# Performance work log

Hardware: AMD Instinct MI355X
Metric: run time of the kernel (lower is better)

## Reference

```python
import jax, jax.numpy as jnp
import numpy as np
from jax.ops import segment_sum

N_NODES = 50000
N_EDGES = 800000
NUM_FEAT = 16
EDGE_DIM = 8
H = 100
L = 2
BN_EPS = 1e-5


def setup_inputs() -> dict:
    key = jax.random.key(0)
    ks = iter(jax.random.split(key, 40))
    def w(shape, scale=0.05):
        return (jax.random.normal(next(ks), shape, dtype=jnp.float32) * scale)
    inp = {
        "x": jax.random.normal(next(ks), (N_NODES, NUM_FEAT), dtype=jnp.float32),
        "edge_index": jax.random.randint(next(ks), (2, N_EDGES), 0, N_NODES, dtype=jnp.int64) if jax.config.jax_enable_x64 else jax.random.randint(next(ks), (2, N_EDGES), 0, N_NODES).astype(jnp.int32),
        "edge_attr": jax.random.normal(next(ks), (N_EDGES, EDGE_DIM), dtype=jnp.float32),
        # embeddings
        "node_w": w((NUM_FEAT, H)), "node_b": w((H,)),
        "edge_w": w((EDGE_DIM, H)), "edge_b": w((H,)),
        # per-layer GINEConv MLP (stacked over layers)
        "conv_w1": w((L, H, H)), "conv_b1": w((L, H)),
        "conv_w2": w((L, H, H)), "conv_b2": w((L, H)),
        # batchnorm affine params
        "bn_gamma": jnp.ones((L, H), dtype=jnp.float32), "bn_beta": jnp.zeros((L, H), dtype=jnp.float32),
        # per-layer edge-update MLP
        "emlp_w1": w((L, 3 * H, H)), "emlp_b1": w((L, H)),
        "emlp_w2": w((L, H, H)), "emlp_b2": w((L, H)),
        # final classifier MLP (3H -> 50 -> 25 -> 2); dropout is identity at eval
        "mlp_w1": w((3 * H, 50)), "mlp_b1": w((50,)),
        "mlp_w2": w((50, 25)), "mlp_b2": w((25,)),
        "mlp_w3": w((25, 2)), "mlp_b3": w((2,)),
    }
    return inp


def reference(x, edge_index, edge_attr,
              node_w, node_b, edge_w, edge_b,
              conv_w1, conv_b1, conv_w2, conv_b2,
              bn_gamma, bn_beta,
              emlp_w1, emlp_b1, emlp_w2, emlp_b2,
              mlp_w1, mlp_b1, mlp_w2, mlp_b2, mlp_w3, mlp_b3):
    src, dst = edge_index[0], edge_index[1]
    n_nodes = x.shape[0]

    h = x @ node_w + node_b          # [N, H]
    e = edge_attr @ edge_w + edge_b  # [E, H]

    for i in range(L):
        # GINEConv: out_i = nn((1+eps)*h_i + sum_{e: dst=i} relu(h_src + e)); eps=0
        msg = jax.nn.relu(h[src] + e)                       # [E, H] gather + combine
        agg = segment_sum(msg, dst, num_segments=n_nodes)   # [N, H] scatter-add
        z = h + agg
        z = jax.nn.relu(z @ conv_w1[i] + conv_b1[i]) @ conv_w2[i] + conv_b2[i]
        # BatchNorm (train mode: batch stats over nodes, biased variance)
        mu = jnp.mean(z, axis=0)
        var = jnp.var(z, axis=0)
        z = (z - mu) * jax.lax.rsqrt(var + BN_EPS) * bn_gamma[i] + bn_beta[i]
        h = (h + jax.nn.relu(z)) * 0.5
        # edge update: e += MLP([h_src, h_dst, e]) / 2
        cat = jnp.concatenate([h[src], h[dst], e], axis=-1)  # [E, 3H]
        upd = jax.nn.relu(cat @ emlp_w1[i] + emlp_b1[i]) @ emlp_w2[i] + emlp_b2[i]
        e = e + upd * 0.5

    # per-edge features: relu([h_src, h_dst]) ++ e  -> [E, 3H]
    feat = jnp.concatenate([jax.nn.relu(jnp.concatenate([h[src], h[dst]], axis=-1)), e], axis=-1)
    out = jax.nn.relu(feat @ mlp_w1 + mlp_b1)
    out = jax.nn.relu(out @ mlp_w2 + mlp_b2)
    return out @ mlp_w3 + mlp_b3  # [E, 2]
```

## Files before the change

kernel.cpp:

```cpp
#include <hip/hip_runtime.h>
#include <hip/hip_bf16.h>

#define N_NODES 50000
#define N_EDGES 800000
#define HDIM 100
#define ESTR 104

typedef _Float16 half8_t __attribute__((ext_vector_type(8)));
typedef _Float16 half4_t __attribute__((ext_vector_type(4)));
typedef float f32x4_t __attribute__((ext_vector_type(4)));

struct FragDesc {
  const float* src; int stride; int K; int N; int outOff; int ksteps; int ntiles;
};
struct PrepArgs {
  FragDesc d[20];
  int prefix[21];
  int ndesc;
};

__global__ void k_prep_frags(PrepArgs args, _Float16* __restrict__ out) {
  int b = blockIdx.x;
  int di = 0;
  while (di + 1 < args.ndesc && b >= args.prefix[di + 1]) di++;
  FragDesc d = args.d[di];
  int local = b - args.prefix[di];
  int t = local / d.ksteps;
  int s = local % d.ksteps;
  int lane = threadIdx.x;
  int col = t * 16 + (lane & 15);
  int kb = s * 32 + (lane >> 4) * 8;
  _Float16* o = out + d.outOff + (size_t)((t * d.ksteps + s) * 64 + lane) * 8;
  #pragma unroll
  for (int i = 0; i < 8; ++i) {
    int k = kb + i;
    float v = (k < d.K && col < d.N) ? d.src[(size_t)k * d.stride + col] : 0.0f;
    o[i] = (_Float16)v;
  }
}

__global__ void k_ws_probe(float* out, float mb) { out[0] = mb; }

__global__ void k_hist(const int* __restrict__ dst, int* __restrict__ cnt) {
  for (int e = blockIdx.x * blockDim.x + threadIdx.x; e < N_EDGES;
       e += gridDim.x * blockDim.x)
    atomicAdd(&cnt[dst[e]], 1);
}

__global__ __launch_bounds__(1024) void k_scan(const int* cnt,
                                               int* rowptr,
                                               int* cursor) {
  __shared__ int part[1024];
  int t = threadIdx.x;
  const int CH = (N_NODES + 1023) / 1024;
  int base = t * CH;
  int s = 0;
  for (int i = 0; i < CH; ++i) {
    int n = base + i;
    if (n < N_NODES) s += cnt[n];
  }
  part[t] = s;
  __syncthreads();
  for (int off = 1; off < 1024; off <<= 1) {
    int v = 0;
    if (t >= off) v = part[t - off];
    __syncthreads();
    if (t >= off) part[t] += v;
    __syncthreads();
  }
  int run = (t == 0) ? 0 : part[t - 1];
  for (int i = 0; i < CH; ++i) {
    int n = base + i;
    if (n <= N_NODES) {
      rowptr[n] = run;
      if (n < N_NODES) {
        int cv = cnt[n];
        cursor[n] = run;
        run += cv;
      }
    }
  }
}

__global__ void k_perm(const int* __restrict__ src, const int* __restrict__ dst,
                       int* __restrict__ cursor, int* __restrict__ perm,
                       int* __restrict__ srcS, int* __restrict__ dstS) {
  for (int e = blockIdx.x * blockDim.x + threadIdx.x; e < N_EDGES;
       e += gridDim.x * blockDim.x) {
    int d = dst[e];
    int pos = atomicAdd(&cursor[d], 1);
    perm[pos] = e;
    srcS[pos] = src[e];
    dstS[pos] = d;
  }
}

template<bool L0>
__global__ __launch_bounds__(256) void k_agg(
    const int* __restrict__ rowptr, const int* __restrict__ perm,
    const int* __restrict__ srcS,
    const float* __restrict__ attr, const float* __restrict__ ew,
    const float* __restrict__ ebias,
    const _Float16* __restrict__ e,
    const float* __restrict__ h, float* __restrict__ agg) {
  __shared__ float EwL[800];
  __shared__ float ebL[128];
  int tid = threadIdx.x;
  if constexpr (L0) {
    for (int idx = tid; idx < 800; idx += 256) EwL[idx] = ew[idx];
    if (tid < 128) ebL[tid] = (tid < HDIM) ? ebias[tid] : 0.0f;
    __syncthreads();
  }
  int n = blockIdx.x * 2 + (tid >> 7);
  int j = tid & 127;
  if (n >= N_NODES || j >= HDIM) return;
  float acc = 0.0f;
  int p0 = rowptr[n], p1 = rowptr[n + 1];
  for (int pos = p0; pos < p1; ++pos) {
    int s = srcS[pos];
    float m;
    if constexpr (L0) {
      int eid = perm[pos];
      const float* ap = attr + (size_t)eid * 8;
      float e0 = ebL[j];
      #pragma unroll
      for (int k = 0; k < 8; ++k) e0 += ap[k] * EwL[k * HDIM + j];
      m = h[(size_t)s * HDIM + j] + e0;
    } else {
      m = h[(size_t)s * HDIM + j] + (float)e[(size_t)pos * ESTR + j];
    }
    acc += fmaxf(m, 0.0f);
  }
  agg[(size_t)n * HDIM + j] = acc;
}

__device__ __forceinline__ half8_t h8_zero() {
  half8_t a;
  #pragma unroll
  for (int i = 0; i < 8; ++i) a[i] = (_Float16)0.0f;
  return a;
}

__device__ __forceinline__ int swz_idx(int r, int c) {
  int chunk = (c >> 3) ^ (r & 7);
  return r * 128 + chunk * 8 + (c & 7);
}

template<int MODE>
__device__ __forceinline__ void load_a_node(const float* hp0,
                                            const float* ap0,
                                            int row, int lane, half8_t av[4]) {
  int g = lane >> 4;
  bool rv = (row < N_NODES);
  const float* hp = hp0 + (size_t)row * HDIM;
  const float* ap = ap0 + (size_t)row * HDIM;
  #pragma unroll
  for (int s = 0; s < 4; ++s) {
    int kb = s * 32 + g * 8;
    half8_t a = h8_zero();
    if (rv && kb < HDIM) {
      float f[8];
      #pragma unroll
      for (int i = 0; i < 8; ++i) f[i] = 0.0f;
      if (kb + 8 <= HDIM) {
        float4 v0 = *(const float4*)(hp + kb);
        float4 v1 = *(const float4*)(hp + kb + 4);
        f[0] = v0.x; f[1] = v0.y; f[2] = v0.z; f[3] = v0.w;
        f[4] = v1.x; f[5] = v1.y; f[6] = v1.z; f[7] = v1.w;
        if constexpr (MODE == 2) {
          float4 u0 = *(const float4*)(ap + kb);
          float4 u1 = *(const float4*)(ap + kb + 4);
          f[0] += u0.x; f[1] += u0.y; f[2] += u0.z; f[3] += u0.w;
          f[4] += u1.x; f[5] += u1.y; f[6] += u1.z; f[7] += u1.w;
        }
      } else {
        float4 v0 = *(const float4*)(hp + kb);
        f[0] = v0.x; f[1] = v0.y; f[2] = v0.z; f[3] = v0.w;
        if constexpr (MODE == 2) {
          float4 u0 = *(const float4*)(ap + kb);
          f[0] += u0.x; f[1] += u0.y; f[2] += u0.z; f[3] += u0.w;
        }
      }
      #pragma unroll
      for (int i = 0; i < 8; ++i) {
        float v = f[i];
        if constexpr (MODE == 1) v = fmaxf(v, 0.0f);
        a[i] = (_Float16)v;
      }
    }
    av[s] = a;
  }
}

template<int NT, int KS>
__device__ __forceinline__ void mfma_tiles(const half8_t* av, const _Float16* __restrict__ fb,
                                           int lane, f32x4_t* acc) {
  #pragma unroll
  for (int t = 0; t < NT; ++t) {
    #pragma unroll
    for (int s = 0; s < KS; ++s) {
      half8_t bv = *(const half8_t*)(fb + (size_t)(((t * KS + s) * 64 + lane) << 3));
      acc[t] = __builtin_amdgcn_mfma_f32_16x16x32_f16(av[s], bv, acc[t], 0, 0, 0);
    }
  }
}

template<int KS>
__device__ __forceinline__ void lds_read_a(const _Float16* L, int lane, half8_t* av) {
  int r = lane & 15;
  int g = lane >> 4;
  #pragma unroll
  for (int s = 0; s < KS; ++s) {
    int kb = s * 32 + g * 8;
    av[s] = *(const half8_t*)&L[swz_idx(r, kb)];
  }
}

__global__ void k_embed_h(const float* __restrict__ x, const float* __restrict__ w,
                          const float* __restrict__ bias, float* __restrict__ h) {
  int n = blockIdx.x;
  int j = threadIdx.x;
  if (j >= HDIM) return;
  float acc = bias[j];
  #pragma unroll
  for (int k = 0; k < 16; ++k) acc += x[n * 16 + k] * w[k * HDIM + j];
  h[(size_t)n * HDIM + j] = acc;
}

__global__ __launch_bounds__(256) void k_node_conv(
    const float* __restrict__ h, const float* agg,
    const _Float16* __restrict__ fb1, const _Float16* __restrict__ fb2,
    const float* __restrict__ b1, const float* __restrict__ b2,
    float* z, float* __restrict__ bn_sum, float* __restrict__ bn_sq) {
  __shared__ __align__(16) _Float16 lds[4][2048];
  int lane = threadIdx.x & 63;
  int wave = threadIdx.x >> 6;
  _Float16* L = lds[wave];
  int mbase = (blockIdx.x * 4 + wave) * 16;

  half8_t av[4];
  load_a_node<2>(h, agg, mbase + (lane & 15), lane, av);
  f32x4_t acc[7];
  #pragma unroll
  for (int t = 0; t < 7; ++t) acc[t] = (f32x4_t){0.f, 0.f, 0.f, 0.f};
  mfma_tiles<7, 4>(av, fb1, lane, acc);

  #pragma unroll
  for (int t = 0; t < 7; ++t) {
    int j = t * 16 + (lane & 15);
    float bias = (j < HDIM) ? b1[j] : 0.0f;
    #pragma unroll
    for (int q = 0; q < 4; ++q) {
      int r = (lane >> 4) * 4 + q;
      float v = fmaxf(acc[t][q] + bias, 0.0f);
      if (j >= HDIM) v = 0.0f;
      L[swz_idx(r, j)] = (_Float16)v;
    }
  }
  { int r = lane >> 2; int c0 = 112 + (lane & 3) * 4;
    #pragma unroll
    for (int i = 0; i < 4; ++i) L[swz_idx(r, c0 + i)] = (_Float16)0.0f;
  }
  __builtin_amdgcn_sched_barrier(0);

  half8_t av2[4];
  lds_read_a<4>(L, lane, av2);
  f32x4_t acc2[7];
  #pragma unroll
  for (int t = 0; t < 7; ++t) acc2[t] = (f32x4_t){0.f, 0.f, 0.f, 0.f};
  mfma_tiles<7, 4>(av2, fb2, lane, acc2);
  __builtin_amdgcn_sched_barrier(0);

  #pragma unroll
  for (int t = 0; t < 7; ++t) {
    int j = t * 16 + (lane & 15);
    float bias = (j < HDIM) ? b2[j] : 0.0f;
    float colsum = 0.0f, colsq = 0.0f;
    #pragma unroll
    for (int q = 0; q < 4; ++q) {
      int row = mbase + (lane >> 4) * 4 + q;
      float v = acc2[t][q] + bias;
      bool ok = (row < N_NODES) && (j < HDIM);
      if (ok) z[(size_t)row * HDIM + j] = v;
      float sv = ok ? v : 0.0f;
      colsum += sv; colsq += sv * sv;
    }
    colsum += __shfl_xor(colsum, 16);
    colsum += __shfl_xor(colsum, 32);
    colsq  += __shfl_xor(colsq, 16);
    colsq  += __shfl_xor(colsq, 32);
    if (lane < 16 && j < HDIM) {
      atomicAdd(&bn_sum[j], colsum);
      atomicAdd(&bn_sq[j], colsq);
    }
  }
}

__global__ void k_bn_final(const float* __restrict__ bn_sum, const float* __restrict__ bn_sq,
                           float* __restrict__ bn_mu, float* __restrict__ bn_rs) {
  int j = threadIdx.x;
  if (j >= HDIM) return;
  float mu = bn_sum[j] / (float)N_NODES;
  float var = bn_sq[j] / (float)N_NODES - mu * mu;
  bn_mu[j] = mu;
  bn_rs[j] = rsqrtf(var + 1e-5f);
}

__global__ __launch_bounds__(256) void k_h_pq(
    float* h, const float* z,
    const float* __restrict__ bn_mu, const float* __restrict__ bn_rs,
    const float* __restrict__ gamma, const float* __restrict__ beta,
    const _Float16* __restrict__ fb, _Float16* __restrict__ PQt) {
  int lane = threadIdx.x & 63;
  int wave = threadIdx.x >> 6;
  int c = lane & 15, g = lane >> 4;
  int mbase = (blockIdx.x * 4 + wave) * 16;
  int row = mbase + c;
  bool rv = row < N_NODES;
  float* hp = h + (size_t)row * HDIM;
  const float* zp = z + (size_t)row * HDIM;

  half8_t av[4];
  #pragma unroll
  for (int s = 0; s < 4; ++s) {
    int kb = s * 32 + g * 8;
    half8_t a = h8_zero();
    if (rv && kb < HDIM) {
      int lim = (kb + 8 <= HDIM) ? 8 : 4;
      float zf[8], hf[8], mu[8], rs[8], ga[8], be[8];
      { float4 v = *(const float4*)(zp + kb);
        zf[0]=v.x; zf[1]=v.y; zf[2]=v.z; zf[3]=v.w; }
      { float4 v = *(const float4*)(hp + kb);
        hf[0]=v.x; hf[1]=v.y; hf[2]=v.z; hf[3]=v.w; }
      { float4 v = *(const float4*)(bn_mu + kb);
        mu[0]=v.x; mu[1]=v.y; mu[2]=v.z; mu[3]=v.w; }
      { float4 v = *(const float4*)(bn_rs + kb);
        rs[0]=v.x; rs[1]=v.y; rs[2]=v.z; rs[3]=v.w; }
      { float4 v = *(const float4*)(gamma + kb);
        ga[0]=v.x; ga[1]=v.y; ga[2]=v.z; ga[3]=v.w; }
      { float4 v = *(const float4*)(beta + kb);
        be[0]=v.x; be[1]=v.y; be[2]=v.z; be[3]=v.w; }
      if (lim == 8) {
        { float4 v = *(const float4*)(zp + kb + 4);
          zf[4]=v.x; zf[5]=v.y; zf[6]=v.z; zf[7]=v.w; }
        { float4 v = *(const float4*)(hp + kb + 4);
          hf[4]=v.x; hf[5]=v.y; hf[6]=v.z; hf[7]=v.w; }
        { float4 v = *(const float4*)(bn_mu + kb + 4);
          mu[4]=v.x; mu[5]=v.y; mu[6]=v.z; mu[7]=v.w; }
        { float4 v = *(const float4*)(bn_rs + kb + 4);
          rs[4]=v.x; rs[5]=v.y; rs[6]=v.z; rs[7]=v.w; }
        { float4 v = *(const float4*)(gamma + kb + 4);
          ga[4]=v.x; ga[5]=v.y; ga[6]=v.z; ga[7]=v.w; }
        { float4 v = *(const float4*)(beta + kb + 4);
          be[4]=v.x; be[5]=v.y; be[6]=v.z; be[7]=v.w; }
      }
      float hn[8];
      #pragma unroll
      for (int i = 0; i < 8; ++i) hn[i] = 0.0f;
      for (int i = 0; i < 8; ++i) {
        if (i < lim) {
          float zn = (zf[i] - mu[i]) * rs[i] * ga[i] + be[i];
          hn[i] = 0.5f * (hf[i] + fmaxf(zn, 0.0f));
          a[i] = (_Float16)hn[i];
        }
      }
      { float4 v; v.x=hn[0]; v.y=hn[1]; v.z=hn[2]; v.w=hn[3];
        *(float4*)(hp + kb) = v; }
      if (lim == 8) {
        float4 v; v.x=hn[4]; v.y=hn[5]; v.z=hn[6]; v.w=hn[7];
        *(float4*)(hp + kb + 4) = v;
      }
    }
    av[s] = a;
  }

  f32x4_t acc[14];
  #pragma unroll
  for (int t = 0; t < 14; ++t) acc[t] = (f32x4_t){0.f, 0.f, 0.f, 0.f};
  mfma_tiles<14, 4>(av, fb, lane, acc);
  #pragma unroll
  for (int q = 0; q < 4; ++q) {
    int orow = mbase + (lane >> 4) * 4 + q;
    if (orow >= N_NODES) continue;
    half8_t hp8, hq8;
    #pragma unroll
    for (int t = 0; t < 8; ++t) {
      hp8[t] = (t < 7) ? (_Float16)acc[t][q] : (_Float16)0.0f;
      hq8[t] = (t < 7) ? (_Float16)acc[7 + t][q] : (_Float16)0.0f;
    }
    *(half8_t*)(PQt + (size_t)orow * 256 + c * 8) = hp8;
    *(half8_t*)(PQt + (size_t)orow * 256 + 128 + c * 8) = hq8;
  }
}

__global__ __launch_bounds__(256) void k_node_rs(const float* __restrict__ h,
                                                 const _Float16* __restrict__ fb,
                                                 _Float16* __restrict__ out) {
  int lane = threadIdx.x & 63;
  int wave = threadIdx.x >> 6;
  int c = lane & 15;
  int mbase = (blockIdx.x * 4 + wave) * 16;
  half8_t av[4];
  load_a_node<1>(h, h, mbase + c, lane, av);
  f32x4_t acc[8];
  #pragma unroll
  for (int t = 0; t < 8; ++t) acc[t] = (f32x4_t){0.f, 0.f, 0.f, 0.f};
  mfma_tiles<8, 4>(av, fb, lane, acc);
  #pragma unroll
  for (int q = 0; q < 4; ++q) {
    int row = mbase + (lane >> 4) * 4 + q;
    if (row >= N_NODES) continue;
    half4_t hr, hs;
    #pragma unroll
    for (int t = 0; t < 4; ++t) {
      hr[t] = (_Float16)acc[t][q];
      hs[t] = (_Float16)acc[4 + t][q];
    }
    *(half4_t*)(out + (size_t)row * 128 + c * 4) = hr;
    *(half4_t*)(out + (size_t)row * 128 + 64 + c * 4) = hs;
  }
}

__global__ __launch_bounds__(256) void k_edge0(
    const float* __restrict__ attr,
    const _Float16* __restrict__ PQ,
    const int* __restrict__ srcS, const int* __restrict__ dstS,
    const int* __restrict__ perm,
    const float* __restrict__ ew, const float* __restrict__ ebias,
    const _Float16* __restrict__ fbW1c, const _Float16* __restrict__ fbW2,
    const float* __restrict__ b1, const float* __restrict__ b2,
    _Float16* __restrict__ e) {
  __shared__ __align__(16) _Float16 lds[4][2048];
  __shared__ float EwL[800];
  __shared__ float ebL[112];
  int tid = threadIdx.x;
  for (int idx = tid; idx < 800; idx += 256) EwL[idx] = ew[idx];
  if (tid < 112) ebL[tid] = (tid < HDIM) ? ebias[tid] : 0.0f;
  __syncthreads();

  int lane = tid & 63;
  int wave = tid >> 6;
  _Float16* L = lds[wave];
  int mbase = (blockIdx.x * 4 + wave) * 16;
  int c = lane & 15, g = lane >> 4;

  int sn[4], dn[4], pv[4];
  #pragma unroll
  for (int q = 0; q < 4; ++q) {
    int row = mbase + g * 4 + q;
    sn[q] = srcS[row]; dn[q] = dstS[row]; pv[q] = perm[row];
  }

  half8_t Pf[4], Qf[4];
  #pragma unroll
  for (int q = 0; q < 4; ++q) {
    Pf[q] = *(const half8_t*)(PQ + (size_t)sn[q] * 256 + c * 8);
    Qf[q] = *(const half8_t*)(PQ + (size_t)dn[q] * 256 + 128 + c * 8);
  }

  float af[4][8];
  #pragma unroll
  for (int q = 0; q < 4; ++q) {
    const float* ap = attr + (size_t)pv[q] * 8;
    float4 a0 = *(const float4*)ap;
    float4 a1 = *(const float4*)(ap + 4);
    af[q][0] = a0.x; af[q][1] = a0.y; af[q][2] = a0.z; af[q][3] = a0.w;
    af[q][4] = a1.x; af[q][5] = a1.y; af[q][6] = a1.z; af[q][7] = a1.w;
  }

  float e0r[7][4];
  #pragma unroll
  for (int t = 0; t < 7; ++t) {
    int j = t * 16 + c;
    #pragma unroll
    for (int q = 0; q < 4; ++q) {
      float v = 0.0f;
      if (j < HDIM) {
        v = ebL[j];
        #pragma unroll
        for (int k = 0; k < 8; ++k) v += af[q][k] * EwL[k * HDIM + j];
      }
      e0r[t][q] = v;
      L[swz_idx(g * 4 + q, j)] = (_Float16)v;
    }
  }
  { int r = lane >> 2; int c0 = 112 + (lane & 3) * 4;
    #pragma unroll
    for (int i = 0; i < 4; ++i) L[swz_idx(r, c0 + i)] = (_Float16)0.0f;
  }
  __builtin_amdgcn_sched_barrier(0);

  half8_t av[4];
  lds_read_a<4>(L, lane, av);
  __builtin_amdgcn_sched_barrier(0);
  f32x4_t acc[7];
  #pragma unroll
  for (int t = 0; t < 7; ++t) acc[t] = (f32x4_t){0.f, 0.f, 0.f, 0.f};
  mfma_tiles<7, 4>(av, fbW1c, lane, acc);

  #pragma unroll
  for (int t = 0; t < 7; ++t) {
    int j = t * 16 + c;
    float bias = (j < HDIM) ? b1[j] : 0.0f;
    #pragma unroll
    for (int q = 0; q < 4; ++q) {
      int r = g * 4 + q;
      float v = 0.0f;
      if (j < HDIM)
        v = fmaxf(acc[t][q] + bias + (float)Pf[q][t] + (float)Qf[q][t], 0.0f);
      L[swz_idx(r, j)] = (_Float16)v;
    }
  }
  __builtin_amdgcn_sched_barrier(0);

  half8_t av2[4];
  lds_read_a<4>(L, lane, av2);
  f32x4_t acc2[7];
  #pragma unroll
  for (int t = 0; t < 7; ++t) acc2[t] = (f32x4_t){0.f, 0.f, 0.f, 0.f};
  mfma_tiles<7, 4>(av2, fbW2, lane, acc2);
  __builtin_amdgcn_sched_barrier(0);

  #pragma unroll
  for (int t = 0; t < 7; ++t) {
    int j = t * 16 + c;
    float b2v = (j < HDIM) ? b2[j] : 0.0f;
    #pragma unroll
    for (int q = 0; q < 4; ++q) {
      int row = mbase + g * 4 + q;
      float eold = (float)(_Float16)e0r[t][q];
      float enew = eold + 0.5f * (acc2[t][q] + b2v);
      if (j < ESTR)
        e[(size_t)row * ESTR + j] = (j < HDIM) ? (_Float16)enew : (_Float16)0.0f;
    }
  }
}

__global__ __launch_bounds__(256) void k_edge1(
    const _Float16* __restrict__ e,
    const _Float16* __restrict__ PQ, const _Float16* __restrict__ RS,
    const int* __restrict__ srcS, const int* __restrict__ dstS,
    const int* __restrict__ perm,
    const _Float16* __restrict__ fbW1c, const _Float16* __restrict__ fbW2,
    const float* __restrict__ b1, const float* __restrict__ b2,
    const _Float16* __restrict__ fbC, const _Float16* __restrict__ fbM2,
    const _Float16* __restrict__ fbM3,
    const float* __restrict__ mb1, const float* __restrict__ mb2,
    const float* __restrict__ mb3, float* __restrict__ out) {
  __shared__ __align__(16) _Float16 lds[4][2048];
  int lane = threadIdx.x & 63;
  int wave = threadIdx.x >> 6;
  _Float16* L = lds[wave];
  int mbase = (blockIdx.x * 4 + wave) * 16;
  int c = lane & 15, g = lane >> 4;

  half8_t av[4];
  {
    const _Float16* ep = e + (size_t)(mbase + c) * ESTR;
    #pragma unroll
    for (int s = 0; s < 3; ++s)
      av[s] = *(const half8_t*)(ep + s * 32 + g * 8);
    av[3] = (g == 0) ? *(const half8_t*)(ep + 96) : h8_zero();
  }

  int sn[4], dn[4];
  #pragma unroll
  for (int q = 0; q < 4; ++q) {
    int row = mbase + g * 4 + q;
    sn[q] = srcS[row]; dn[q] = dstS[row];
  }
  half8_t Pf[4], Qf[4];
  #pragma unroll
  for (int q = 0; q < 4; ++q) {
    Pf[q] = *(const half8_t*)(PQ + (size_t)sn[q] * 256 + c * 8);
    Qf[q] = *(const half8_t*)(PQ + (size_t)dn[q] * 256 + 128 + c * 8);
  }

  f32x4_t acc[7];
  #pragma unroll
  for (int t = 0; t < 7; ++t) acc[t] = (f32x4_t){0.f, 0.f, 0.f, 0.f};
  mfma_tiles<7, 4>(av, fbW1c, lane, acc);

  #pragma unroll
  for (int t = 0; t < 7; ++t) {
    int j = t * 16 + c;
    float bias = (j < HDIM) ? b1[j] : 0.0f;
    #pragma unroll
    for (int q = 0; q < 4; ++q) {
      int r = g * 4 + q;
      float v = 0.0f;
      if (j < HDIM)
        v = fmaxf(acc[t][q] + bias + (float)Pf[q][t] + (float)Qf[q][t], 0.0f);
      L[swz_idx(r, j)] = (_Float16)v;
    }
  }
  { int r = lane >> 2; int c0 = 112 + (lane & 3) * 4;
    #pragma unroll
    for (int i = 0; i < 4; ++i) L[swz_idx(r, c0 + i)] = (_Float16)0.0f;
  }
  __builtin_amdgcn_sched_barrier(0);

  half4_t Rf[4], Sf[4];
  #pragma unroll
  for (int q = 0; q < 4; ++q) {
    Rf[q] = *(const half4_t*)(RS + (size_t)sn[q] * 128 + c * 4);
    Sf[q] = *(const half4_t*)(RS + (size_t)dn[q] * 128 + 64 + c * 4);
  }

  half8_t av2[4];
  lds_read_a<4>(L, lane, av2);
  f32x4_t acc2[7];
  #pragma unroll
  for (int t = 0; t < 7; ++t) acc2[t] = (f32x4_t){0.f, 0.f, 0.f, 0.f};
  mfma_tiles<7, 4>(av2, fbW2, lane, acc2);
  __builtin_amdgcn_sched_barrier(0);

  #pragma unroll
  for (int t = 0; t < 7; ++t) {
    int j = t * 16 + c;
    float bias = (j < HDIM) ? b2[j] : 0.0f;
    #pragma unroll
    for (int q = 0; q < 4; ++q) {
      int row = mbase + g * 4 + q;
      float v = 0.0f;
      if (j < HDIM) {
        float eold = (float)e[(size_t)row * ESTR + j];
        v = eold + 0.5f * (acc2[t][q] + bias);
      }
      int r = g * 4 + q;
      L[swz_idx(r, j)] = (_Float16)v;
    }
  }
  __builtin_amdgcn_sched_barrier(0);

  half8_t av3[4];
  lds_read_a<4>(L, lane, av3);
  f32x4_t acc3[4];
  #pragma unroll
  for (int t = 0; t < 4; ++t) acc3[t] = (f32x4_t){0.f, 0.f, 0.f, 0.f};
  mfma_tiles<4, 4>(av3, fbC, lane, acc3);
  __builtin_amdgcn_sched_barrier(0);
  #pragma unroll
  for (int t = 0; t < 4; ++t) {
    int j = t * 16 + c;
    float bias = (j < 50) ? mb1[j] : 0.0f;
    #pragma unroll
    for (int q = 0; q < 4; ++q) {
      float v = 0.0f;
      if (j < 50)
        v = fmaxf(acc3[t][q] + bias + (float)Rf[q][t] + (float)Sf[q][t], 0.0f);
      int r = g * 4 + q;
      L[swz_idx(r, j)] = (_Float16)v;
    }
  }
  __builtin_amdgcn_sched_barrier(0);
  half8_t av4[2];
  lds_read_a<2>(L, lane, av4);
  f32x4_t acc4[2];
  #pragma unroll
  for (int t = 0; t < 2; ++t) acc4[t] = (f32x4_t){0.f, 0.f, 0.f, 0.f};
  mfma_tiles<2, 2>(av4, fbM2, lane, acc4);
  __builtin_amdgcn_sched_barrier(0);
  #pragma unroll
  for (int t = 0; t < 2; ++t) {
    int j = t * 16 + c;
    float bias = (j < 25) ? mb2[j] : 0.0f;
    #pragma unroll
    for (int q = 0; q < 4; ++q) {
      float v = (j < 25) ? fmaxf(acc4[t][q] + bias, 0.0f) : 0.0f;
      int r = g * 4 + q;
      L[swz_idx(r, j)] = (_Float16)v;
    }
  }
  __builtin_amdgcn_sched_barrier(0);
  half8_t av5[1];
  lds_read_a<1>(L, lane, av5);
  f32x4_t acc5 = (f32x4_t){0.f, 0.f, 0.f, 0.f};
  {
    half8_t bv = *(const half8_t*)(fbM3 + (size_t)(lane << 3));
    acc5 = __builtin_amdgcn_mfma_f32_16x16x32_f16(av5[0], bv, acc5, 0, 0, 0);
  }
  if (c < 2) {
    float bias = mb3[c];
    #pragma unroll
    for (int q = 0; q < 4; ++q) {
      int row = mbase + g * 4 + q;
      out[(size_t)perm[row] * 2 + c] = acc5[q] + bias;
    }
  }
}

extern "C" void kernel_launch(void* const* d_in, const int* in_sizes, int n_in,
                              void* d_out, int out_size, void* d_ws, size_t ws_size,
                              hipStream_t stream) {
  const float* x        = (const float*)d_in[0];
  const int*   ei       = (const int*)  d_in[1];
  const float* eattr    = (const float*)d_in[2];
  const float* node_w   = (const float*)d_in[3];
  const float* node_b   = (const float*)d_in[4];
  const float* edge_w   = (const float*)d_in[5];
  const float* edge_b   = (const float*)d_in[6];
  const float* conv_w1  = (const float*)d_in[7];
  const float* conv_b1  = (const float*)d_in[8];
  const float* conv_w2  = (const float*)d_in[9];
  const float* conv_b2  = (const float*)d_in[10];
  const float* bn_gamma = (const float*)d_in[11];
  const float* bn_beta  = (const float*)d_in[12];
  const float* emlp_w1  = (const float*)d_in[13];
  const float* emlp_b1  = (const float*)d_in[14];
  const float* emlp_w2  = (const float*)d_in[15];
  const float* emlp_b2  = (const float*)d_in[16];
  const float* mlp_w1   = (const float*)d_in[17];
  const float* mlp_b1   = (const float*)d_in[18];
  const float* mlp_w2   = (const float*)d_in[19];
  const float* mlp_b2   = (const float*)d_in[20];
  const float* mlp_w3   = (const float*)d_in[21];
  const float* mlp_b3   = (const float*)d_in[22];
  const int* src = ei;
  const int* dst = ei + N_EDGES;

  char* ws = (char*)d_ws;
  size_t off = 0;
  auto alloc = [&](size_t bytes) -> void* {
    void* p = ws + off;
    off += (bytes + 255) & ~(size_t)255;
    return p;
  };
  _Float16* e    = (_Float16*)alloc((size_t)N_EDGES * ESTR * 2);
  float* h       = (float*)alloc((size_t)N_NODES * HDIM * 4);
  float* agg     = (float*)alloc((size_t)N_NODES * HDIM * 4);
  _Float16* PQt  = (_Float16*)alloc((size_t)N_NODES * 256 * 2);
  int* cursor    = (int*)alloc((size_t)N_NODES * 4);
  int* rowptr    = (int*)alloc((size_t)(N_NODES + 1) * 4);
  int* perm      = (int*)alloc((size_t)N_EDGES * 4);
  int* srcS      = (int*)alloc((size_t)N_EDGES * 4);
  int* dstS      = (int*)alloc((size_t)N_EDGES * 4);
  float* bn_sum  = (float*)alloc(512);
  float* bn_sq   = (float*)alloc(512);
  float* bn_mu   = (float*)alloc(512);
  float* bn_rs   = (float*)alloc(512);
  _Float16* frags = (_Float16*)alloc(200000 * 2);
  float* z = agg;
  _Float16* RSt = (_Float16*)agg;

  if (off > ws_size) {
    k_ws_probe<<<1, 1, 0, stream>>>((float*)d_out, (float)(ws_size >> 20));
    return;
  }

  PrepArgs pa;
  int nd = 0, tilesum = 0, fo = 0;
  auto add = [&](const float* sp, int stride, int K, int Ncols, int ksteps, int ntiles) -> int {
    pa.d[nd] = FragDesc{sp, stride, K, Ncols, fo, ksteps, ntiles};
    pa.prefix[nd] = tilesum;
    tilesum += ksteps * ntiles;
    ++nd;
    int ret = fo;
    fo += ksteps * ntiles * 512;
    return ret;
  };
  int offConvW1[2], offConvW2[2], offPQ[2], offW1c[2], offW2e[2];
  for (int i = 0; i < 2; ++i) {
    offConvW1[i] = add(conv_w1 + i * 10000, 100, 100, 100, 4, 7);
    offConvW2[i] = add(conv_w2 + i * 10000, 100, 100, 100, 4, 7);
    offPQ[i]     = add(emlp_w1 + i * 30000,         100, 100, 100, 4, 7);
                   add(emlp_w1 + i * 30000 + 10000, 100, 100, 100, 4, 7);
    offW1c[i]    = add(emlp_w1 + i * 30000 + 20000, 100, 100, 100, 4, 7);
    offW2e[i]    = add(emlp_w2 + i * 10000, 100, 100, 100, 4, 7);
  }
  int offRS = add(mlp_w1,         50, 100, 50, 4, 4);
              add(mlp_w1 + 5000,  50, 100, 50, 4, 4);
  int offC  = add(mlp_w1 + 10000, 50, 100, 50, 4, 4);
  int offM2 = add(mlp_w2, 25, 50, 25, 2, 2);
  int offM3 = add(mlp_w3, 2, 25, 2, 1, 1);
  pa.prefix[nd] = tilesum;
  pa.ndesc = nd;

  hipMemsetAsync(cursor, 0, (size_t)N_NODES * 4, stream);
  k_hist<<<2048, 256, 0, stream>>>(dst, cursor);
  k_scan<<<1, 1024, 0, stream>>>(cursor, rowptr, cursor);
  k_perm<<<2048, 256, 0, stream>>>(src, dst, cursor, perm, srcS, dstS);

  k_prep_frags<<<tilesum, 64, 0, stream>>>(pa, frags);
  k_embed_h<<<N_NODES, 128, 0, stream>>>(x, node_w, node_b, h);
  k_agg<true><<<N_NODES / 2, 256, 0, stream>>>(rowptr, perm, srcS,
                                               eattr, edge_w, edge_b,
                                               nullptr, h, agg);

  const int nodeGrid = (N_NODES + 63) / 64;
  for (int i = 0; i < 2; ++i) {
    hipMemsetAsync(bn_sum, 0, 512, stream);
    hipMemsetAsync(bn_sq, 0, 512, stream);
    k_node_conv<<<nodeGrid, 256, 0, stream>>>(h, agg, frags + offConvW1[i], frags + offConvW2[i],
                                              conv_b1 + i * 100, conv_b2 + i * 100,
                                              z, bn_sum, bn_sq);
    k_bn_final<<<1, 128, 0, stream>>>(bn_sum, bn_sq, bn_mu, bn_rs);
    k_h_pq<<<nodeGrid, 256, 0, stream>>>(h, z, bn_mu, bn_rs,
                                         bn_gamma + i * 100, bn_beta + i * 100,
                                         frags + offPQ[i], PQt);
    if (i == 0) {
      k_edge0<<<N_EDGES / 64, 256, 0, stream>>>(
          eattr, PQt, srcS, dstS, perm, edge_w, edge_b,
          frags + offW1c[0], frags + offW2e[0],
          emlp_b1, emlp_b2, e);
      k_agg<false><<<N_NODES / 2, 256, 0, stream>>>(rowptr, perm, srcS,
                                                    nullptr, nullptr, nullptr,
                                                    e, h, agg);
    } else {
      k_node_rs<<<nodeGrid, 256, 0, stream>>>(h, frags + offRS, RSt);
      k_edge1<<<N_EDGES / 64, 256, 0, stream>>>(
          e, PQt, RSt, srcS, dstS, perm,
          frags + offW1c[1], frags + offW2e[1],
          emlp_b1 + 100, emlp_b2 + 100,
          frags + offC, frags + offM2, frags + offM3,
          mlp_b1, mlp_b2, mlp_b3, (float*)d_out);
    }
  }
}
```

Measured before the change: 1.505 ms.

## Gather fp16 node features in aggregation and process two edge tiles per wave

Adds an fp16 copy of node features, padded to a stride of 104 and written by the embed and h_pq kernels, so the edge aggregation gathers half-width rows instead of fp32 rows. Separately, the final edge kernel now has each wave handle two 16-edge tiles, with all gathers for both tiles issued up front, and launches half as many blocks. The fp16 gather is meant to cut gather bandwidth, and the two-tile loop is meant to overlap gather latency with MFMA work. In exchange it needs an extra workspace buffer, adds rounding of h before aggregation, and raises register pressure in the edge kernel.

Result: slower. 1.745 ms (+16.0%).

```diff
diff --git a/kernel.cpp b/kernel.cpp
--- a/kernel.cpp
+++ b/kernel.cpp
@@ -102,7 +102,8 @@
     const float* __restrict__ attr, const float* __restrict__ ew,
     const float* __restrict__ ebias,
     const _Float16* __restrict__ e,
-    const float* __restrict__ h, float* __restrict__ agg) {
+    const float* __restrict__ h, const _Float16* __restrict__ h16,
+    float* __restrict__ agg) {
   __shared__ float EwL[800];
   __shared__ float ebL[128];
   int tid = threadIdx.x;
@@ -118,6 +119,7 @@
   int p0 = rowptr[n], p1 = rowptr[n + 1];
   for (int pos = p0; pos < p1; ++pos) {
     int s = srcS[pos];
+    float hv = h16 ? (float)h16[(size_t)s * 104 + j] : h[(size_t)s * HDIM + j];
     float m;
     if constexpr (L0) {
       int eid = perm[pos];
@@ -125,9 +127,9 @@
       float e0 = ebL[j];
       #pragma unroll
       for (int k = 0; k < 8; ++k) e0 += ap[k] * EwL[k * HDIM + j];
-      m = h[(size_t)s * HDIM + j] + e0;
+      m = hv + e0;
     } else {
-      m = h[(size_t)s * HDIM + j] + (float)e[(size_t)pos * ESTR + j];
+      m = hv + (float)e[(size_t)pos * ESTR + j];
     }
     acc += fmaxf(m, 0.0f);
   }
@@ -217,14 +219,19 @@
 }
 
 __global__ void k_embed_h(const float* __restrict__ x, const float* __restrict__ w,
-                          const float* __restrict__ bias, float* __restrict__ h) {
+                          const float* __restrict__ bias, float* __restrict__ h,
+                          _Float16* __restrict__ h16) {
   int n = blockIdx.x;
   int j = threadIdx.x;
-  if (j >= HDIM) return;
-  float acc = bias[j];
-  #pragma unroll
-  for (int k = 0; k < 16; ++k) acc += x[n * 16 + k] * w[k * HDIM + j];
-  h[(size_t)n * HDIM + j] = acc;
+  float acc = 0.0f;
+  if (j < HDIM) {
+    acc = bias[j];
+    #pragma unroll
+    for (int k = 0; k < 16; ++k) acc += x[n * 16 + k] * w[k * HDIM + j];
+    h[(size_t)n * HDIM + j] = acc;
+  }
+  if (h16 && j < 104)
+    h16[(size_t)n * 104 + j] = (j < HDIM) ? (_Float16)acc : (_Float16)0.0f;
 }
 
 __global__ __launch_bounds__(256) void k_node_conv(
@@ -310,7 +317,8 @@
     float* h, const float* z,
     const float* __restrict__ bn_mu, const float* __restrict__ bn_rs,
     const float* __restrict__ gamma, const float* __restrict__ beta,
-    const _Float16* __restrict__ fb, _Float16* __restrict__ PQt) {
+    const _Float16* __restrict__ fb, _Float16* __restrict__ PQt,
+    _Float16* __restrict__ h16) {
   int lane = threadIdx.x & 63;
   int wave = threadIdx.x >> 6;
   int c = lane & 15, g = lane >> 4;
@@ -370,6 +378,8 @@
         float4 v; v.x=hn[4]; v.y=hn[5]; v.z=hn[6]; v.w=hn[7];
         *(float4*)(hp + kb + 4) = v;
       }
+      if (h16)
+        *(half8_t*)(h16 + (size_t)row * 104 + kb) = a;
     }
     av[s] = a;
   }
@@ -536,6 +546,135 @@
   }
 }
 
+__device__ __forceinline__ void edge1_body(
+    const _Float16* __restrict__ e,
+    const _Float16* __restrict__ RS,
+    const int* sn, const int* dn, const int* __restrict__ perm,
+    int mbase, int lane, _Float16* L,
+    const half8_t* av, const half8_t* Pf, const half8_t* Qf,
+    const _Float16* __restrict__ fbW1c, const _Float16* __restrict__ fbW2,
+    const float* __restrict__ b1, const float* __restrict__ b2,
+    const _Float16* __restrict__ fbC, const _Float16* __restrict__ fbM2,
+    const _Float16* __restrict__ fbM3,
+    const float* __restrict__ mb1, const float* __restrict__ mb2,
+    const float* __restrict__ mb3, float* __restrict__ out) {
+  int c = lane & 15, g = lane >> 4;
+
+  f32x4_t acc[7];
+  #pragma unroll
+  for (int t = 0; t < 7; ++t) acc[t] = (f32x4_t){0.f, 0.f, 0.f, 0.f};
+  mfma_tiles<7, 4>(av, fbW1c, lane, acc);
+
+  #pragma unroll
+  for (int t = 0; t < 7; ++t) {
+    int j = t * 16 + c;
+    float bias = (j < HDIM) ? b1[j] : 0.0f;
+    #pragma unroll
+    for (int q = 0; q < 4; ++q) {
+      int r = g * 4 + q;
+      float v = 0.0f;
+      if (j < HDIM)
+        v = fmaxf(acc[t][q] + bias + (float)Pf[q][t] + (float)Qf[q][t], 0.0f);
+      L[swz_idx(r, j)] = (_Float16)v;
+    }
+  }
+  { int r = lane >> 2; int c0 = 112 + (lane & 3) * 4;
+    #pragma unroll
+    for (int i = 0; i < 4; ++i) L[swz_idx(r, c0 + i)] = (_Float16)0.0f;
+  }
+  __builtin_amdgcn_sched_barrier(0);
+
+  half4_t Rf[4], Sf[4];
+  #pragma unroll
+  for (int q = 0; q < 4; ++q) {
+    Rf[q] = *(const half4_t*)(RS + (size_t)sn[q] * 128 + c * 4);
+    Sf[q] = *(const half4_t*)(RS + (size_t)dn[q] * 128 + 64 + c * 4);
+  }
+
+  half8_t av2[4];
+  lds_read_a<4>(L, lane, av2);
+  f32x4_t acc2[7];
+  #pragma unroll
+  for (int t = 0; t < 7; ++t) acc2[t] = (f32x4_t){0.f, 0.f, 0.f, 0.f};
+  mfma_tiles<7, 4>(av2, fbW2, lane, acc2);
+  __builtin_amdgcn_sched_barrier(0);
+
+  #pragma unroll
+  for (int t = 0; t < 7; ++t) {
+    int j = t * 16 + c;
+    float bias = (j < HDIM) ? b2[j] : 0.0f;
+    #pragma unroll
+    for (int q = 0; q < 4; ++q) {
+      int row = mbase + g * 4 + q;
+      float v = 0.0f;
+      if (j < HDIM) {
+        float eold = (float)e[(size_t)row * ESTR + j];
+        v = eold + 0.5f * (acc2[t][q] + bias);
+      }
+      int r = g * 4 + q;
+      L[swz_idx(r, j)] = (_Float16)v;
+    }
+  }
+  __builtin_amdgcn_sched_barrier(0);
+
+  half8_t av3[4];
+  lds_read_a<4>(L, lane, av3);
+  f32x4_t acc3[4];
+  #pragma unroll
+  for (int t = 0; t < 4; ++t) acc3[t] = (f32x4_t){0.f, 0.f, 0.f, 0.f};
+  mfma_tiles<4, 4>(av3, fbC, lane, acc3);
+  __builtin_amdgcn_sched_barrier(0);
+  #pragma unroll
+  for (int t = 0; t < 4; ++t) {
+    int j = t * 16 + c;
+    float bias = (j < 50) ? mb1[j] : 0.0f;
+    #pragma unroll
+    for (int q = 0; q < 4; ++q) {
+      float v = 0.0f;
+      if (j < 50)
+        v = fmaxf(acc3[t][q] + bias + (float)Rf[q][t] + (float)Sf[q][t], 0.0f);
+      int r = g * 4 + q;
+      L[swz_idx(r, j)] = (_Float16)v;
+    }
+  }
+  __builtin_amdgcn_sched_barrier(0);
+  half8_t av4[2];
+  lds_read_a<2>(L, lane, av4);
+  f32x4_t acc4[2];
+  #pragma unroll
+  for (int t = 0; t < 2; ++t) acc4[t] = (f32x4_t){0.f, 0.f, 0.f, 0.f};
+  mfma_tiles<2, 2>(av4, fbM2, lane, acc4);
+  __builtin_amdgcn_sched_barrier(0);
+  #pragma unroll
+  for (int t = 0; t < 2; ++t) {
+    int j = t * 16 + c;
+    float bias = (j < 25) ? mb2[j] : 0.0f;
+    #pragma unroll
+    for (int q = 0; q < 4; ++q) {
+      float v = (j < 25) ? fmaxf(acc4[t][q] + bias, 0.0f) : 0.0f;
+      int r = g * 4 + q;
+      L[swz_idx(r, j)] = (_Float16)v;
+    }
+  }
+  __builtin_amdgcn_sched_barrier(0);
+  half8_t av5[1];
+  lds_read_a<1>(L, lane, av5);
+  f32x4_t acc5 = (f32x4_t){0.f, 0.f, 0.f, 0.f};
+  {
+    half8_t bv = *(const half8_t*)(fbM3 + (size_t)(lane << 3));
+    acc5 = __builtin_amdgcn_mfma_f32_16x16x32_f16(av5[0], bv, acc5, 0, 0, 0);
+  }
+  if (c < 2) {
+    float bias = mb3[c];
+    #pragma unroll
+    for (int q = 0; q < 4; ++q) {
+      int row = mbase + g * 4 + q;
+      out[(size_t)perm[row] * 2 + c] = acc5[q] + bias;
+    }
+  }
+  __builtin_amdgcn_sched_barrier(0);
+}
+
 __global__ __launch_bounds__(256) void k_edge1(
     const _Float16* __restrict__ e,
     const _Float16* __restrict__ PQ, const _Float16* __restrict__ RS,
@@ -551,143 +690,44 @@
   int lane = threadIdx.x & 63;
   int wave = threadIdx.x >> 6;
   _Float16* L = lds[wave];
-  int mbase = (blockIdx.x * 4 + wave) * 16;
+  int mbA = (blockIdx.x * 8 + wave * 2) * 16;
+  int mbB = mbA + 16;
   int c = lane & 15, g = lane >> 4;
 
-  half8_t av[4];
+  half8_t avA[4], avB[4];
   {
-    const _Float16* ep = e + (size_t)(mbase + c) * ESTR;
-    #pragma unroll
-    for (int s = 0; s < 3; ++s)
-      av[s] = *(const half8_t*)(ep + s * 32 + g * 8);
-    av[3] = (g == 0) ? *(const half8_t*)(ep + 96) : h8_zero();
-  }
-
-  int sn[4], dn[4];
+    const _Float16* ep = e + (size_t)(mbA + c) * ESTR;
+    #pragma unroll
+    for (int s = 0; s < 3; ++s) avA[s] = *(const half8_t*)(ep + s * 32 + g * 8);
+    avA[3] = (g == 0) ? *(const half8_t*)(ep + 96) : h8_zero();
+  }
+  {
+    const _Float16* ep = e + (size_t)(mbB + c) * ESTR;
+    #pragma unroll
+    for (int s = 0; s < 3; ++s) avB[s] = *(const half8_t*)(ep + s * 32 + g * 8);
+    avB[3] = (g == 0) ? *(const half8_t*)(ep + 96) : h8_zero();
+  }
+
+  int snA[4], dnA[4], snB[4], dnB[4];
   #pragma unroll
   for (int q = 0; q < 4; ++q) {
-    int row = mbase + g * 4 + q;
-    sn[q] = srcS[row]; dn[q] = dstS[row];
-  }
-  half8_t Pf[4], Qf[4];
+    int rA = mbA + g * 4 + q, rB = mbB + g * 4 + q;
+    snA[q] = srcS[rA]; dnA[q] = dstS[rA];
+    snB[q] = srcS[rB]; dnB[q] = dstS[rB];
+  }
+  half8_t PfA[4], QfA[4], PfB[4], QfB[4];
   #pragma unroll
   for (int q = 0; q < 4; ++q) {
-    Pf[q] = *(const half8_t*)(PQ + (size_t)sn[q] * 256 + c * 8);
-    Qf[q] = *(const half8_t*)(PQ + (size_t)dn[q] * 256 + 128 + c * 8);
-  }
-
-  f32x4_t acc[7];
-  #pragma unroll
-  for (int t = 0; t < 7; ++t) acc[t] = (f32x4_t){0.f, 0.f, 0.f, 0.f};
-  mfma_tiles<7, 4>(av, fbW1c, lane, acc);
-
-  #pragma unroll
-  for (int t = 0; t < 7; ++t) {
-    int j = t * 16 + c;
-    float bias = (j < HDIM) ? b1[j] : 0.0f;
-    #pragma unroll
-    for (int q = 0; q < 4; ++q) {
-      int r = g * 4 + q;
-      float v = 0.0f;
-      if (j < HDIM)
-        v = fmaxf(acc[t][q] + bias + (float)Pf[q][t] + (float)Qf[q][t], 0.0f);
-      L[swz_idx(r, j)] = (_Float16)v;
-    }
-  }
-  { int r = lane >> 2; int c0 = 112 + (lane & 3) * 4;
-    #pragma unroll
-    for (int i = 0; i < 4; ++i) L[swz_idx(r, c0 + i)] = (_Float16)0.0f;
-  }
-  __builtin_amdgcn_sched_barrier(0);
-
-  half4_t Rf[4], Sf[4];
-  #pragma unroll
-  for (int q = 0; q < 4; ++q) {
-    Rf[q] = *(const half4_t*)(RS + (size_t)sn[q] * 128 + c * 4);
-    Sf[q] = *(const half4_t*)(RS + (size_t)dn[q] * 128 + 64 + c * 4);
-  }
-
-  half8_t av2[4];
-  lds_read_a<4>(L, lane, av2);
-  f32x4_t acc2[7];
-  #pragma unroll
-  for (int t = 0; t < 7; ++t) acc2[t] = (f32x4_t){0.f, 0.f, 0.f, 0.f};
-  mfma_tiles<7, 4>(av2, fbW2, lane, acc2);
-  __builtin_amdgcn_sched_barrier(0);
-
-  #pragma unroll
-  for (int t = 0; t < 7; ++t) {
-    int j = t * 16 + c;
-    float bias = (j < HDIM) ? b2[j] : 0.0f;
-    #pragma unroll
-    for (int q = 0; q < 4; ++q) {
-      int row = mbase + g * 4 + q;
-      float v = 0.0f;
-      if (j < HDIM) {
-        float eold = (float)e[(size_t)row * ESTR + j];
-        v = eold + 0.5f * (acc2[t][q] + bias);
-      }
-      int r = g * 4 + q;
-      L[swz_idx(r, j)] = (_Float16)v;
-    }
-  }
-  __builtin_amdgcn_sched_barrier(0);
-
-  half8_t av3[4];
-  lds_read_a<4>(L, lane, av3);
-  f32x4_t acc3[4];
-  #pragma unroll
-  for (int t = 0; t < 4; ++t) acc3[t] = (f32x4_t){0.f, 0.f, 0.f, 0.f};
-  mfma_tiles<4, 4>(av3, fbC, lane, acc3);
-  __builtin_amdgcn_sched_barrier(0);
-  #pragma unroll
-  for (int t = 0; t < 4; ++t) {
-    int j = t * 16 + c;
-    float bias = (j < 50) ? mb1[j] : 0.0f;
-    #pragma unroll
-    for (int q = 0; q < 4; ++q) {
-      float v = 0.0f;
-      if (j < 50)
-        v = fmaxf(acc3[t][q] + bias + (float)Rf[q][t] + (float)Sf[q][t], 0.0f);
-      int r = g * 4 + q;
-      L[swz_idx(r, j)] = (_Float16)v;
-    }
-  }
-  __builtin_amdgcn_sched_barrier(0);
-  half8_t av4[2];
-  lds_read_a<2>(L, lane, av4);
-  f32x4_t acc4[2];
-  #pragma unroll
-  for (int t = 0; t < 2; ++t) acc4[t] = (f32x4_t){0.f, 0.f, 0.f, 0.f};
-  mfma_tiles<2, 2>(av4, fbM2, lane, acc4);
-  __builtin_amdgcn_sched_barrier(0);
-  #pragma unroll
-  for (int t = 0; t < 2; ++t) {
-    int j = t * 16 + c;
-    float bias = (j < 25) ? mb2[j] : 0.0f;
-    #pragma unroll
-    for (int q = 0; q < 4; ++q) {
-      float v = (j < 25) ? fmaxf(acc4[t][q] + bias, 0.0f) : 0.0f;
-      int r = g * 4 + q;
-      L[swz_idx(r, j)] = (_Float16)v;
-    }
-  }
-  __builtin_amdgcn_sched_barrier(0);
-  half8_t av5[1];
-  lds_read_a<1>(L, lane, av5);
-  f32x4_t acc5 = (f32x4_t){0.f, 0.f, 0.f, 0.f};
-  {
-    half8_t bv = *(const half8_t*)(fbM3 + (size_t)(lane << 3));
-    acc5 = __builtin_amdgcn_mfma_f32_16x16x32_f16(av5[0], bv, acc5, 0, 0, 0);
-  }
-  if (c < 2) {
-    float bias = mb3[c];
-    #pragma unroll
-    for (int q = 0; q < 4; ++q) {
-      int row = mbase + g * 4 + q;
-      out[(size_t)perm[row] * 2 + c] = acc5[q] + bias;
-    }
-  }
+    PfA[q] = *(const half8_t*)(PQ + (size_t)snA[q] * 256 + c * 8);
+    QfA[q] = *(const half8_t*)(PQ + (size_t)dnA[q] * 256 + 128 + c * 8);
+    PfB[q] = *(const half8_t*)(PQ + (size_t)snB[q] * 256 + c * 8);
+    QfB[q] = *(const half8_t*)(PQ + (size_t)dnB[q] * 256 + 128 + c * 8);
+  }
+
+  edge1_body(e, RS, snA, dnA, perm, mbA, lane, L, avA, PfA, QfA,
+             fbW1c, fbW2, b1, b2, fbC, fbM2, fbM3, mb1, mb2, mb3, out);
+  edge1_body(e, RS, snB, dnB, perm, mbB, lane, L, avB, PfB, QfB,
+             fbW1c, fbW2, b1, b2, fbC, fbM2, fbM3, mb1, mb2, mb3, out);
 }
 
 extern "C" void kernel_launch(void* const* d_in, const int* in_sizes, int n_in,
@@ -748,6 +788,10 @@
     return;
   }
 
+  size_t off_save = off;
+  _Float16* h16 = (_Float16*)alloc((size_t)N_NODES * 104 * 2);
+  if (off > ws_size) { h16 = nullptr; off = off_save; }
+
   PrepArgs pa;
   int nd = 0, tilesum = 0, fo = 0;
   auto add = [&](const float* sp, int stride, int K, int Ncols, int ksteps, int ntiles) -> int {
@@ -782,10 +826,10 @@
   k_perm<<<2048, 256, 0, stream>>>(src, dst, cursor, perm, srcS, dstS);
 
   k_prep_frags<<<tilesum, 64, 0, stream>>>(pa, frags);
-  k_embed_h<<<N_NODES, 128, 0, stream>>>(x, node_w, node_b, h);
+  k_embed_h<<<N_NODES, 128, 0, stream>>>(x, node_w, node_b, h, h16);
   k_agg<true><<<N_NODES / 2, 256, 0, stream>>>(rowptr, perm, srcS,
                                                eattr, edge_w, edge_b,
-                                               nullptr, h, agg);
+                                               nullptr, h, h16, agg);
 
   const int nodeGrid = (N_NODES + 63) / 64;
   for (int i = 0; i < 2; ++i) {
@@ -797,7 +841,8 @@
     k_bn_final<<<1, 128, 0, stream>>>(bn_sum, bn_sq, bn_mu, bn_rs);
     k_h_pq<<<nodeGrid, 256, 0, stream>>>(h, z, bn_mu, bn_rs,
                                          bn_gamma + i * 100, bn_beta + i * 100,
-                                         frags + offPQ[i], PQt);
+                                         frags + offPQ[i], PQt,
+                                         (i == 0) ? h16 : nullptr);
     if (i == 0) {
       k_edge0<<<N_EDGES / 64, 256, 0, stream>>>(
           eattr, PQt, srcS, dstS, perm, edge_w, edge_b,
@@ -805,10 +850,10 @@
           emlp_b1, emlp_b2, e);
       k_agg<false><<<N_NODES / 2, 256, 0, stream>>>(rowptr, perm, srcS,
                                                     nullptr, nullptr, nullptr,
-                                                    e, h, agg);
+                                                    e, h, h16, agg);
     } else {
       k_node_rs<<<nodeGrid, 256, 0, stream>>>(h, frags + offRS, RSt);
-      k_edge1<<<N_EDGES / 64, 256, 0, stream>>>(
+      k_edge1<<<N_EDGES / 128, 256, 0, stream>>>(
           e, PQt, RSt, srcS, dstS, perm,
           frags + offW1c[1], frags + offW2e[1],
           emlp_b1 + 100, emlp_b2 + 100,
```
